# Kernel optimization log

Hardware: AMD Instinct MI355X
Metric: run time of the kernel (lower is better)

The kernel has to match this reference:

```python
import jax, jax.numpy as jnp
import numpy as np

N_NODES = 100000
N_EDGES = 1600000
IN_DIM = 128
HID = 32
HEADS = 4
NEG_SLOPE = 0.2


def gat_conv(x, src, dst, W, att_src, att_dst, bias, n_nodes, heads, out_ch):
    # x: [N, Fin], W: [Fin, heads*out_ch], att_*: [heads, out_ch], bias: [heads*out_ch]
    h = (x @ W).reshape(n_nodes, heads, out_ch)            # [N, H, C]
    a_src = jnp.einsum('nhc,hc->nh', h, att_src)           # [N, H]
    a_dst = jnp.einsum('nhc,hc->nh', h, att_dst)           # [N, H]
    e = jax.nn.leaky_relu(a_src[src] + a_dst[dst], NEG_SLOPE)  # [E, H]
    # segment softmax over incoming edges of each target node
    e_max = jax.ops.segment_max(e, dst, num_segments=n_nodes)  # [N, H]
    ex = jnp.exp(e - e_max[dst])                               # [E, H]
    denom = jax.ops.segment_sum(ex, dst, num_segments=n_nodes)  # [N, H]
    alpha = ex / denom[dst]                                     # [E, H]
    msg = h[src] * alpha[:, :, None]                            # [E, H, C]
    out = jax.ops.segment_sum(msg, dst, num_segments=n_nodes)   # [N, H, C]
    return out.reshape(n_nodes, heads * out_ch) + bias


def setup_inputs() -> dict:
    key = jax.random.key(0)
    ks = jax.random.split(key, 10)
    x = jax.random.normal(ks[0], (N_NODES, IN_DIM), dtype=jnp.float32)
    edge_index = jax.random.randint(ks[1], (2, N_EDGES), 0, N_NODES, dtype=jnp.int64) if jax.config.jax_enable_x64 else jax.random.randint(ks[1], (2, N_EDGES), 0, N_NODES, dtype=jnp.int32)
    s = 0.1
    W1 = jax.random.normal(ks[2], (IN_DIM, HEADS * HID), dtype=jnp.float32) * s
    att_src1 = jax.random.normal(ks[3], (HEADS, HID), dtype=jnp.float32) * s
    att_dst1 = jax.random.normal(ks[4], (HEADS, HID), dtype=jnp.float32) * s
    b1 = jnp.zeros((HEADS * HID,), dtype=jnp.float32)
    W2 = jax.random.normal(ks[5], (HEADS * HID, HEADS * HID), dtype=jnp.float32) * s
    att_src2 = jax.random.normal(ks[6], (HEADS, HID), dtype=jnp.float32) * s
    att_dst2 = jax.random.normal(ks[7], (HEADS, HID), dtype=jnp.float32) * s
    b2 = jnp.zeros((HEADS * HID,), dtype=jnp.float32)
    return {"x": x, "edge_index": edge_index, "W1": W1, "att_src1": att_src1,
            "att_dst1": att_dst1, "b1": b1, "W2": W2, "att_src2": att_src2,
            "att_dst2": att_dst2, "b2": b2}


def reference(x, edge_index, W1, att_src1, att_dst1, b1, W2, att_src2, att_dst2, b2):
    src, dst = edge_index[0], edge_index[1]
    x1 = jax.nn.relu(gat_conv(x, src, dst, W1, att_src1, att_dst1, b1, N_NODES, HEADS, HID))
    x2 = jax.nn.relu(gat_conv(x1, src, dst, W2, att_src2, att_dst2, b2, N_NODES, HEADS, HID))
    # [N, heads*hid, 2]
    return jnp.concatenate([x1[:, :, None], x2[:, :, None]], axis=2)
```

## Files before the change

### kernel.cpp

```cpp
#include <hip/hip_runtime.h>

#define NN 100000
#define NE 1600000
#define GEMM_GRID 1563
#define NBUK 391
#define BCAP 5120
#define PA_BLOCKS 320
#define PA_EDGES 5000
#define K1_GRID (16 + PA_BLOCKS)
#define K2_GRID (NBUK + GEMM_GRID)
#define AG1_GRID 6250
#define AGG2_GRID 12500

typedef short bf16x8 __attribute__((ext_vector_type(8)));
typedef float f32x4 __attribute__((ext_vector_type(4)));
typedef unsigned int u32;
typedef u32 u32x4 __attribute__((ext_vector_type(4)));
typedef unsigned short u16;

__device__ inline u32 bf16r(float x) {
    u32 u = __float_as_uint(x);
    return (u + 0x7FFFu + ((u >> 16) & 1u)) >> 16;
}

__device__ inline void split_pack8(const float a[8], u32 hh[4], u32 ll[4]) {
#pragma unroll
    for (int j = 0; j < 4; ++j) {
        u32 u0 = __float_as_uint(a[2 * j]);
        u32 u1 = __float_as_uint(a[2 * j + 1]);
        float l0 = a[2 * j] - __uint_as_float(u0 & 0xFFFF0000u);
        float l1 = a[2 * j + 1] - __uint_as_float(u1 & 0xFFFF0000u);
        hh[j] = (u0 >> 16) | (u1 & 0xFFFF0000u);
        ll[j] = (__float_as_uint(l0) >> 16) | (__float_as_uint(l1) & 0xFFFF0000u);
    }
}

__device__ inline void wpack_body(int idx, const float* __restrict__ W,
                                  bf16x8* __restrict__ wpH, bf16x8* __restrict__ wpL) {
    if (idx >= 2048) return;
    int lane = idx & 63, tile = idx >> 6;
    int kc = tile >> 3, ct = tile & 7;
    int col = lane & 15, kq = lane >> 4;
    int kbase = kc * 32 + kq * 8;
    float a[8];
#pragma unroll
    for (int i = 0; i < 8; ++i)
        a[i] = W[(size_t)(kbase + i) * 128 + ct * 16 + col];
    u32 hh[4], ll[4];
    split_pack8(a, hh, ll);
    wpH[tile * 64 + lane] = __builtin_bit_cast(bf16x8, (u32x4){hh[0], hh[1], hh[2], hh[3]});
    wpL[tile * 64 + lane] = __builtin_bit_cast(bf16x8, (u32x4){ll[0], ll[1], ll[2], ll[3]});
}

__global__ __launch_bounds__(256) void k1(
    const float* __restrict__ W1, bf16x8* __restrict__ wpH1, bf16x8* __restrict__ wpL1,
    const float* __restrict__ W2, bf16x8* __restrict__ wpH2, bf16x8* __restrict__ wpL2,
    const int* __restrict__ dst, const int* __restrict__ src,
    int* __restrict__ gtail, u32* __restrict__ tmp) {
    const int b = blockIdx.x;
    if (b < 8) {
        wpack_body(b * 256 + threadIdx.x, W1, wpH1, wpL1);
        return;
    } else if (b < 16) {
        wpack_body((b - 8) * 256 + threadIdx.x, W2, wpH2, wpL2);
        return;
    }
    __shared__ int lhist[NBUK], lcur[NBUK];
    const int t = threadIdx.x;
    const int e0 = (b - 16) * PA_EDGES;
    const int e1 = e0 + PA_EDGES;
    for (int i = t; i < NBUK; i += 256) lhist[i] = 0;
    __syncthreads();
    for (int e = e0 + t; e < e1; e += 256)
        atomicAdd(&lhist[dst[e] >> 8], 1);
    __syncthreads();
    for (int i = t; i < NBUK; i += 256)
        if (lhist[i] > 0) lcur[i] = atomicAdd(&gtail[i], lhist[i]);
    __syncthreads();
    for (int e = e0 + t; e < e1; e += 256) {
        int d = dst[e];
        int bb = d >> 8;
        int p = atomicAdd(&lcur[bb], 1);
        tmp[(size_t)bb * BCAP + p] = ((u32)(d & 255) << 17) | (u32)src[e];
    }
}

__device__ inline void gemm_epilogue(f32x4 acc[8], int row0, int w, int col, int kq,
                                     const float* __restrict__ atts,
                                     const float* __restrict__ attd,
                                     u16* __restrict__ hb,
                                     float* __restrict__ a_src,
                                     float* __restrict__ a_dst) {
    float as0[4], as1[4], ad0[4], ad1[4];
#pragma unroll
    for (int q = 0; q < 4; ++q) {
        as0[q] = atts[q * 32 + col];
        as1[q] = atts[q * 32 + 16 + col];
        ad0[q] = attd[q * 32 + col];
        ad1[q] = attd[q * 32 + 16 + col];
    }
#pragma unroll
    for (int r = 0; r < 4; ++r) {
        int node = row0 + w * 16 + kq * 4 + r;
        float ps[4], pd[4];
#pragma unroll
        for (int q = 0; q < 4; ++q) {
            float d0 = acc[2 * q][r], d1 = acc[2 * q + 1][r];
            ps[q] = d0 * as0[q] + d1 * as1[q];
            pd[q] = d0 * ad0[q] + d1 * ad1[q];
        }
#pragma unroll
        for (int off = 1; off < 16; off <<= 1) {
#pragma unroll
            for (int q = 0; q < 4; ++q) {
                ps[q] += __shfl_xor(ps[q], off);
                pd[q] += __shfl_xor(pd[q], off);
            }
        }
        if (node < NN) {
#pragma unroll
            for (int ct = 0; ct < 8; ++ct)
                hb[(size_t)node * 128 + ct * 16 + col] = (u16)bf16r(acc[ct][r]);
            if (col < 4) {
                float vs = col == 0 ? ps[0] : col == 1 ? ps[1] : col == 2 ? ps[2] : ps[3];
                float vd = col == 0 ? pd[0] : col == 1 ? pd[1] : col == 2 ? pd[2] : pd[3];
                a_src[node * 4 + col] = vs;
                a_dst[node * 4 + col] = vd;
            }
        }
    }
}

__global__ __launch_bounds__(256) void k2(
    const float* __restrict__ x,
    const bf16x8* __restrict__ wpH, const bf16x8* __restrict__ wpL,
    const float* __restrict__ atts, const float* __restrict__ attd,
    u16* __restrict__ hb, float* __restrict__ a_src, float* __restrict__ a_dst,
    const int* __restrict__ gtail, const u32* __restrict__ tmp,
    int* __restrict__ row_ptr, int* __restrict__ src_sorted) {
    __shared__ u32 ldata[BCAP];
    __shared__ int lh[256];
    __shared__ int lsc[256];
    const int idx = blockIdx.x;
    const int t = threadIdx.x;
    if (idx < NBUK) {
        const int g = idx;
        const int n = gtail[g];
        int acc = 0;
        for (int i = t; i < g; i += 256) acc += gtail[i];
        lsc[t] = acc;
        __syncthreads();
        for (int off = 128; off > 0; off >>= 1) {
            if (t < off) lsc[t] += lsc[t + off];
            __syncthreads();
        }
        const int ebase = lsc[0];
        lh[t] = 0;
        __syncthreads();
        for (int i = t; i < n; i += 256) {
            u32 v = tmp[(size_t)g * BCAP + i];
            ldata[i] = v;
            atomicAdd(&lh[v >> 17], 1);
        }
        __syncthreads();
        int c = lh[t];
        lsc[t] = c;
        __syncthreads();
        for (int off = 1; off < 256; off <<= 1) {
            int xv = (t >= off) ? lsc[t - off] : 0;
            __syncthreads();
            lsc[t] += xv;
            __syncthreads();
        }
        int excl = (t == 0) ? 0 : lsc[t - 1];
        int base = ebase + excl;
        lh[t] = base;
        int node = (g << 8) + t;
        if (node < NN) row_ptr[node] = base;
        if (g == NBUK - 1 && t == 0) row_ptr[NN] = ebase + n;
        __syncthreads();
        for (int i = t; i < n; i += 256) {
            u32 v = ldata[i];
            int p = atomicAdd(&lh[v >> 17], 1);
            src_sorted[p] = (int)(v & 0x1FFFFu);
        }
        return;
    }
    const int row0 = (idx - NBUK) * 64;
    const int lane = t & 63;
    const int w = t >> 6;
    const int col = lane & 15, kq = lane >> 4;
    int node_a = row0 + w * 16 + col;
    if (node_a > NN - 1) node_a = NN - 1;
    const float* xrow = x + (size_t)node_a * 128 + kq * 8;
    float a[32];
#pragma unroll
    for (int kc = 0; kc < 4; ++kc) {
        *(float4*)&a[kc * 8 + 0] = *(const float4*)(xrow + kc * 32);
        *(float4*)&a[kc * 8 + 4] = *(const float4*)(xrow + kc * 32 + 4);
    }
    f32x4 acc[8];
#pragma unroll
    for (int ct = 0; ct < 8; ++ct) acc[ct] = (f32x4){0.f, 0.f, 0.f, 0.f};
#pragma unroll
    for (int kc = 0; kc < 4; ++kc) {
        u32 hh[4], ll[4];
        split_pack8(&a[kc * 8], hh, ll);
        bf16x8 ah = __builtin_bit_cast(bf16x8, (u32x4){hh[0], hh[1], hh[2], hh[3]});
        bf16x8 al = __builtin_bit_cast(bf16x8, (u32x4){ll[0], ll[1], ll[2], ll[3]});
#pragma unroll
        for (int ct = 0; ct < 8; ++ct) {
            bf16x8 bh = wpH[(kc * 8 + ct) * 64 + lane];
            bf16x8 bl = wpL[(kc * 8 + ct) * 64 + lane];
            acc[ct] = __builtin_amdgcn_mfma_f32_16x16x32_bf16(ah, bh, acc[ct], 0, 0, 0);
            acc[ct] = __builtin_amdgcn_mfma_f32_16x16x32_bf16(al, bh, acc[ct], 0, 0, 0);
            acc[ct] = __builtin_amdgcn_mfma_f32_16x16x32_bf16(ah, bl, acc[ct], 0, 0, 0);
        }
    }
    gemm_epilogue(acc, row0, w, col, kq, atts, attd, hb, a_src, a_dst);
}

__global__ __launch_bounds__(256) void k_ag1(
    const u32* __restrict__ hb,
    const float* __restrict__ a_src, const float* __restrict__ a_dst,
    const int* __restrict__ row_ptr, const int* __restrict__ src_sorted,
    const float* __restrict__ bias1,
    const bf16x8* __restrict__ wpH2, const bf16x8* __restrict__ wpL2,
    const float* __restrict__ atts2, const float* __restrict__ attd2,
    u32* __restrict__ x1b, u16* __restrict__ hb2,
    float* __restrict__ a_src2, float* __restrict__ a_dst2) {
    __shared__ __align__(16) u32 xs[16][68];
    const int t = threadIdx.x;
    const int lane = t & 63;
    const int wv = t >> 6;
    const int q = lane >> 4;
    const int es = lane & 15;
    const int hbase = lane & 48;
    const int node0 = blockIdx.x * 16;
    const float bv0 = bias1[lane * 2], bv1 = bias1[lane * 2 + 1];
#pragma unroll 1
    for (int ni = 0; ni < 4; ++ni) {
        const int node = node0 + wv * 4 + ni;
        const int e0 = row_ptr[node], e1 = row_ptr[node + 1];
        const int emax = e1 - 1;
        const float advh = a_dst[node * 4 + q];
        float den = 0.f, a0a = 0.f, a0b = 0.f, a1a = 0.f, a1b = 0.f;
        if (e1 > e0) {
            int eidx = e0 + es;
            if (eidx > emax) eidx = emax;
            int sv = src_sorted[eidx];
            float av = a_src[sv * 4 + q];
            for (int ec = e0; ec < e1; ec += 16) {
                int cnt = e1 - ec;
                cnt = cnt < 16 ? cnt : 16;
                int eidxn = ec + 16 + es;
                if (eidxn > emax) eidxn = emax;
                int svn = src_sorted[eidxn];
                float avn = a_src[svn * 4 + q];
                float lk = av + advh;
                lk = lk > 0.f ? lk : 0.2f * lk;
                float ex = (es < cnt) ? __expf(lk - 8.f) : 0.f;
                den += ex;
                if (cnt == 16) {
                    u32 wvv[16];
#pragma unroll
                    for (int u = 0; u < 16; ++u) {
                        int su = __builtin_amdgcn_readlane(sv, u);
                        wvv[u] = hb[((size_t)su << 6) + lane];
                    }
                    float exu[16];
#pragma unroll
                    for (int u = 0; u < 16; ++u) exu[u] = __shfl(ex, hbase | u);
#pragma unroll
                    for (int u = 0; u < 16; ++u) {
                        float h0 = __uint_as_float(wvv[u] << 16);
                        float h1 = __uint_as_float(wvv[u] & 0xFFFF0000u);
                        if (u & 1) { a0b = fmaf(exu[u], h0, a0b); a1b = fmaf(exu[u], h1, a1b); }
                        else       { a0a = fmaf(exu[u], h0, a0a); a1a = fmaf(exu[u], h1, a1a); }
                    }
                } else {
                    for (int u0 = 0; u0 < cnt; u0 += 4) {
                        u32 wvv[4];
                        float exu[4];
#pragma unroll
                        for (int j = 0; j < 4; ++j) {
                            int su = __builtin_amdgcn_readlane(sv, u0 + j);
                            wvv[j] = hb[((size_t)su << 6) + lane];
                        }
#pragma unroll
                        for (int j = 0; j < 4; ++j) exu[j] = __shfl(ex, hbase | (u0 + j));
#pragma unroll
                        for (int j = 0; j < 4; ++j) {
                            float h0 = __uint_as_float(wvv[j] << 16);
                            float h1 = __uint_as_float(wvv[j] & 0xFFFF0000u);
                            if (j & 1) { a0b = fmaf(exu[j], h0, a0b); a1b = fmaf(exu[j], h1, a1b); }
                            else       { a0a = fmaf(exu[j], h0, a0a); a1a = fmaf(exu[j], h1, a1a); }
                        }
                    }
                }
                sv = svn;
                av = avn;
            }
        }
        float a0 = a0a + a0b, a1 = a1a + a1b;
#pragma unroll
        for (int m = 1; m < 16; m <<= 1) den += __shfl_xor(den, m);
        float inv = den > 0.f ? 1.f / den : 0.f;
        float r0 = fmaxf(fmaf(a0, inv, bv0), 0.f);
        float r1 = fmaxf(fmaf(a1, inv, bv1), 0.f);
        u32 pair = bf16r(r0) | (bf16r(r1) << 16);
        x1b[node * 64 + lane] = pair;
        xs[wv * 4 + ni][lane] = pair;
    }
    __syncthreads();
    const int col = lane & 15, kq = lane >> 4;
    const int ct0 = 2 * wv, ct1 = 2 * wv + 1;
    int4 aw[4];
#pragma unroll
    for (int kc = 0; kc < 4; ++kc)
        aw[kc] = *(const int4*)&xs[col][kc * 16 + kq * 4];
    f32x4 acc0 = (f32x4){0.f, 0.f, 0.f, 0.f};
    f32x4 acc1 = (f32x4){0.f, 0.f, 0.f, 0.f};
#pragma unroll
    for (int kc = 0; kc < 4; ++kc) {
        bf16x8 a = __builtin_bit_cast(bf16x8, aw[kc]);
        acc0 = __builtin_amdgcn_mfma_f32_16x16x32_bf16(a, wpH2[(kc * 8 + ct0) * 64 + lane], acc0, 0, 0, 0);
        acc0 = __builtin_amdgcn_mfma_f32_16x16x32_bf16(a, wpL2[(kc * 8 + ct0) * 64 + lane], acc0, 0, 0, 0);
        acc1 = __builtin_amdgcn_mfma_f32_16x16x32_bf16(a, wpH2[(kc * 8 + ct1) * 64 + lane], acc1, 0, 0, 0);
        acc1 = __builtin_amdgcn_mfma_f32_16x16x32_bf16(a, wpL2[(kc * 8 + ct1) * 64 + lane], acc1, 0, 0, 0);
    }
    const float as0 = atts2[wv * 32 + col], as1 = atts2[wv * 32 + 16 + col];
    const float ad0 = attd2[wv * 32 + col], ad1 = attd2[wv * 32 + 16 + col];
#pragma unroll
    for (int r = 0; r < 4; ++r) {
        int node = node0 + kq * 4 + r;
        float d0 = acc0[r], d1 = acc1[r];
        float ps = d0 * as0 + d1 * as1;
        float pd = d0 * ad0 + d1 * ad1;
#pragma unroll
        for (int off = 1; off < 16; off <<= 1) {
            ps += __shfl_xor(ps, off);
            pd += __shfl_xor(pd, off);
        }
        hb2[(size_t)node * 128 + ct0 * 16 + col] = (u16)bf16r(d0);
        hb2[(size_t)node * 128 + ct1 * 16 + col] = (u16)bf16r(d1);
        if (col == 0) {
            a_src2[node * 4 + wv] = ps;
            a_dst2[node * 4 + wv] = pd;
        }
    }
}

__global__ __launch_bounds__(256, 4) void k_agg2(
    const u32* __restrict__ hb,
    const float* __restrict__ a_src, const float* __restrict__ a_dst,
    const int* __restrict__ row_ptr, const int* __restrict__ src_sorted,
    const float* __restrict__ bias,
    const u32* __restrict__ x1b, float* __restrict__ outp) {
    const int lane = threadIdx.x & 63;
    const int node0 = blockIdx.x * 8 + (threadIdx.x >> 6) * 2;
    const int q = lane >> 4;
    const int es = lane & 15;
    const int hbase = lane & 48;
#pragma unroll
    for (int ni = 0; ni < 2; ++ni) {
        const int node = node0 + ni;
        if (node >= NN) continue;
        const int e0 = row_ptr[node], e1 = row_ptr[node + 1];
        const int emax = e1 - 1;
        const float advh = a_dst[node * 4 + q];
        float den = 0.f, a0a = 0.f, a0b = 0.f, a1a = 0.f, a1b = 0.f;
        if (e1 > e0) {
            int eidx = e0 + es;
            if (eidx > emax) eidx = emax;
            int sv = src_sorted[eidx];
            float av = a_src[sv * 4 + q];
            for (int ec = e0; ec < e1; ec += 16) {
                int cnt = e1 - ec;
                cnt = cnt < 16 ? cnt : 16;
                int eidxn = ec + 16 + es;
                if (eidxn > emax) eidxn = emax;
                int svn = src_sorted[eidxn];
                float avn = a_src[svn * 4 + q];
                float lk = av + advh;
                lk = lk > 0.f ? lk : 0.2f * lk;
                float ex = (es < cnt) ? __expf(lk - 8.f) : 0.f;
                den += ex;
                if (cnt == 16) {
                    u32 wv[16];
#pragma unroll
                    for (int u = 0; u < 16; ++u) {
                        int su = __builtin_amdgcn_readlane(sv, u);
                        wv[u] = hb[((size_t)su << 6) + lane];
                    }
                    float exu[16];
#pragma unroll
                    for (int u = 0; u < 16; ++u) exu[u] = __shfl(ex, hbase | u);
#pragma unroll
                    for (int u = 0; u < 16; ++u) {
                        float h0 = __uint_as_float(wv[u] << 16);
                        float h1 = __uint_as_float(wv[u] & 0xFFFF0000u);
                        if (u & 1) { a0b = fmaf(exu[u], h0, a0b); a1b = fmaf(exu[u], h1, a1b); }
                        else       { a0a = fmaf(exu[u], h0, a0a); a1a = fmaf(exu[u], h1, a1a); }
                    }
                } else {
                    for (int u0 = 0; u0 < cnt; u0 += 4) {
                        u32 wv[4];
                        float exu[4];
#pragma unroll
                        for (int j = 0; j < 4; ++j) {
                            int su = __builtin_amdgcn_readlane(sv, u0 + j);
                            wv[j] = hb[((size_t)su << 6) + lane];
                        }
#pragma unroll
                        for (int j = 0; j < 4; ++j) exu[j] = __shfl(ex, hbase | (u0 + j));
#pragma unroll
                        for (int j = 0; j < 4; ++j) {
                            float h0 = __uint_as_float(wv[j] << 16);
                            float h1 = __uint_as_float(wv[j] & 0xFFFF0000u);
                            if (j & 1) { a0b = fmaf(exu[j], h0, a0b); a1b = fmaf(exu[j], h1, a1b); }
                            else       { a0a = fmaf(exu[j], h0, a0a); a1a = fmaf(exu[j], h1, a1a); }
                        }
                    }
                }
                sv = svn;
                av = avn;
            }
        }
        float a0 = a0a + a0b, a1 = a1a + a1b;
#pragma unroll
        for (int m = 1; m < 16; m <<= 1) den += __shfl_xor(den, m);
        float inv = den > 0.f ? 1.f / den : 0.f;
        int c0 = lane * 2;
        float r0 = fmaxf(fmaf(a0, inv, bias[c0]), 0.f);
        float r1 = fmaxf(fmaf(a1, inv, bias[c0 + 1]), 0.f);
        u32 w1 = x1b[node * 64 + lane];
        float4 o;
        o.x = __uint_as_float(w1 << 16);
        o.y = r0;
        o.z = __uint_as_float(w1 & 0xFFFF0000u);
        o.w = r1;
        u32x4 ov = __builtin_bit_cast(u32x4, o);
        __builtin_nontemporal_store(ov,
            (u32x4*)(outp + (size_t)node * 256 + lane * 4));
    }
}


extern "C" void kernel_launch(void* const* d_in, const int* in_sizes, int n_in,
                              void* d_out, int out_size, void* d_ws, size_t ws_size,
                              hipStream_t stream) {
    const float* x   = (const float*)d_in[0];
    const int*   ei  = (const int*)d_in[1];
    const float* W1  = (const float*)d_in[2];
    const float* as1 = (const float*)d_in[3];
    const float* ad1 = (const float*)d_in[4];
    const float* b1  = (const float*)d_in[5];
    const float* W2  = (const float*)d_in[6];
    const float* as2 = (const float*)d_in[7];
    const float* ad2 = (const float*)d_in[8];
    const float* b2  = (const float*)d_in[9];
    float* out = (float*)d_out;
    const int* src = ei;
    const int* dst = ei + NE;

    char* w = (char*)d_ws;
    size_t off = 0;
    auto alloc = [&](size_t bytes) -> void* {
        void* p = w + off;
        off = (off + bytes + 255) & ~((size_t)255);
        return p;
    };
    u16* hb         = (u16*)alloc((size_t)NN * 128 * 2);
    u16* hb2        = (u16*)alloc((size_t)NN * 128 * 2);
    u32* x1b        = (u32*)alloc((size_t)NN * 64 * 4);
    float* a_src    = (float*)alloc((size_t)NN * 4 * 4);
    float* a_dst    = (float*)alloc((size_t)NN * 4 * 4);
    float* a_src2   = (float*)alloc((size_t)NN * 4 * 4);
    float* a_dst2   = (float*)alloc((size_t)NN * 4 * 4);
    int* row_ptr    = (int*)alloc((size_t)(NN + 1) * 4);
    int* gtail      = (int*)alloc(NBUK * 4);
    u32* tmp        = (u32*)alloc((size_t)NBUK * BCAP * 4);
    int* src_sorted = (int*)alloc((size_t)NE * 4);
    bf16x8* wpH1    = (bf16x8*)alloc(2048 * 16);
    bf16x8* wpL1    = (bf16x8*)alloc(2048 * 16);
    bf16x8* wpH2    = (bf16x8*)alloc(2048 * 16);
    bf16x8* wpL2    = (bf16x8*)alloc(2048 * 16);

    (void)hipMemsetAsync(gtail, 0, NBUK * 4, stream);
    k1<<<K1_GRID, 256, 0, stream>>>(W1, wpH1, wpL1, W2, wpH2, wpL2,
                                    dst, src, gtail, tmp);
    k2<<<K2_GRID, 256, 0, stream>>>(x, wpH1, wpL1, as1, ad1, hb, a_src, a_dst,
                                    gtail, tmp, row_ptr, src_sorted);
    k_ag1<<<AG1_GRID, 256, 0, stream>>>((const u32*)hb, a_src, a_dst, row_ptr,
                                        src_sorted, b1, wpH2, wpL2, as2, ad2,
                                        x1b, hb2, a_src2, a_dst2);
    k_agg2<<<AGG2_GRID, 256, 0, stream>>>((const u32*)hb2, a_src2, a_dst2,
                                          row_ptr, src_sorted, b2,
                                          (const u32*)x1b, out);
}
```

Baseline: 248.4 us.

## Make layer-2 GEMM in k_ag1 per-wave to drop block barrier

Each wave now computes the layer-2 projection for its own 4 nodes across all 8 column tiles, using a private shared-memory slice, instead of the block's 4 waves splitting column tiles over 16 shared nodes. This replaces __syncthreads with a wave-local LDS wait, so waves with short neighbor lists no longer stall on slower ones. The cost is 4x the MFMA work per wave, since 12 of the 16 MFMA rows are duplicated padding. It also means 8 accumulators, more registers, and only a quarter of lanes doing stores.

```diff
diff --git a/kernel.cpp b/kernel.cpp
--- a/kernel.cpp
+++ b/kernel.cpp
@@ -229,18 +229,18 @@
     const float* __restrict__ atts2, const float* __restrict__ attd2,
     u32* __restrict__ x1b, u16* __restrict__ hb2,
     float* __restrict__ a_src2, float* __restrict__ a_dst2) {
-    __shared__ __align__(16) u32 xs[16][68];
+    __shared__ __align__(16) u32 xs[4][16][68];
     const int t = threadIdx.x;
     const int lane = t & 63;
     const int wv = t >> 6;
     const int q = lane >> 4;
     const int es = lane & 15;
     const int hbase = lane & 48;
-    const int node0 = blockIdx.x * 16;
+    const int node0 = blockIdx.x * 16 + wv * 4;
     const float bv0 = bias1[lane * 2], bv1 = bias1[lane * 2 + 1];
 #pragma unroll 1
     for (int ni = 0; ni < 4; ++ni) {
-        const int node = node0 + wv * 4 + ni;
+        const int node = node0 + ni;
         const int e0 = row_ptr[node], e1 = row_ptr[node + 1];
         const int emax = e1 - 1;
         const float advh = a_dst[node * 4 + q];
@@ -310,43 +310,63 @@
         float r1 = fmaxf(fmaf(a1, inv, bv1), 0.f);
         u32 pair = bf16r(r0) | (bf16r(r1) << 16);
         x1b[node * 64 + lane] = pair;
-        xs[wv * 4 + ni][lane] = pair;
-    }
-    __syncthreads();
+        xs[wv][ni][lane] = pair;
+    }
+    asm volatile("s_waitcnt lgkmcnt(0)" ::: "memory");
+    __builtin_amdgcn_sched_barrier(0);
     const int col = lane & 15, kq = lane >> 4;
-    const int ct0 = 2 * wv, ct1 = 2 * wv + 1;
     int4 aw[4];
 #pragma unroll
     for (int kc = 0; kc < 4; ++kc)
-        aw[kc] = *(const int4*)&xs[col][kc * 16 + kq * 4];
-    f32x4 acc0 = (f32x4){0.f, 0.f, 0.f, 0.f};
-    f32x4 acc1 = (f32x4){0.f, 0.f, 0.f, 0.f};
+        aw[kc] = *(const int4*)&xs[wv][col & 3][kc * 16 + kq * 4];
+    f32x4 acc[8];
+#pragma unroll
+    for (int ct = 0; ct < 8; ++ct) acc[ct] = (f32x4){0.f, 0.f, 0.f, 0.f};
 #pragma unroll
     for (int kc = 0; kc < 4; ++kc) {
         bf16x8 a = __builtin_bit_cast(bf16x8, aw[kc]);
-        acc0 = __builtin_amdgcn_mfma_f32_16x16x32_bf16(a, wpH2[(kc * 8 + ct0) * 64 + lane], acc0, 0, 0, 0);
-        acc0 = __builtin_amdgcn_mfma_f32_16x16x32_bf16(a, wpL2[(kc * 8 + ct0) * 64 + lane], acc0, 0, 0, 0);
-        acc1 = __builtin_amdgcn_mfma_f32_16x16x32_bf16(a, wpH2[(kc * 8 + ct1) * 64 + lane], acc1, 0, 0, 0);
-        acc1 = __builtin_amdgcn_mfma_f32_16x16x32_bf16(a, wpL2[(kc * 8 + ct1) * 64 + lane], acc1, 0, 0, 0);
-    }
-    const float as0 = atts2[wv * 32 + col], as1 = atts2[wv * 32 + 16 + col];
-    const float ad0 = attd2[wv * 32 + col], ad1 = attd2[wv * 32 + 16 + col];
+#pragma unroll
+        for (int ct = 0; ct < 8; ++ct) {
+            acc[ct] = __builtin_amdgcn_mfma_f32_16x16x32_bf16(a, wpH2[(kc * 8 + ct) * 64 + lane], acc[ct], 0, 0, 0);
+            acc[ct] = __builtin_amdgcn_mfma_f32_16x16x32_bf16(a, wpL2[(kc * 8 + ct) * 64 + lane], acc[ct], 0, 0, 0);
+        }
+    }
+    float as0[4], as1[4], ad0[4], ad1[4];
+#pragma unroll
+    for (int qq = 0; qq < 4; ++qq) {
+        as0[qq] = atts2[qq * 32 + col];
+        as1[qq] = atts2[qq * 32 + 16 + col];
+        ad0[qq] = attd2[qq * 32 + col];
+        ad1[qq] = attd2[qq * 32 + 16 + col];
+    }
 #pragma unroll
     for (int r = 0; r < 4; ++r) {
-        int node = node0 + kq * 4 + r;
-        float d0 = acc0[r], d1 = acc1[r];
-        float ps = d0 * as0 + d1 * as1;
-        float pd = d0 * ad0 + d1 * ad1;
+        int node = node0 + r;
+        float ps[4], pd[4];
+#pragma unroll
+        for (int qq = 0; qq < 4; ++qq) {
+            float d0 = acc[2 * qq][r], d1 = acc[2 * qq + 1][r];
+            ps[qq] = d0 * as0[qq] + d1 * as1[qq];
+            pd[qq] = d0 * ad0[qq] + d1 * ad1[qq];
+        }
 #pragma unroll
         for (int off = 1; off < 16; off <<= 1) {
-            ps += __shfl_xor(ps, off);
-            pd += __shfl_xor(pd, off);
-        }
-        hb2[(size_t)node * 128 + ct0 * 16 + col] = (u16)bf16r(d0);
-        hb2[(size_t)node * 128 + ct1 * 16 + col] = (u16)bf16r(d1);
-        if (col == 0) {
-            a_src2[node * 4 + wv] = ps;
-            a_dst2[node * 4 + wv] = pd;
+#pragma unroll
+            for (int qq = 0; qq < 4; ++qq) {
+                ps[qq] += __shfl_xor(ps[qq], off);
+                pd[qq] += __shfl_xor(pd[qq], off);
+            }
+        }
+        if (kq == 0) {
+#pragma unroll
+            for (int ct = 0; ct < 8; ++ct)
+                hb2[(size_t)node * 128 + ct * 16 + col] = (u16)bf16r(acc[ct][r]);
+            if (col < 4) {
+                float vs = col == 0 ? ps[0] : col == 1 ? ps[1] : col == 2 ? ps[2] : ps[3];
+                float vd = col == 0 ? pd[0] : col == 1 ? pd[1] : col == 2 ? pd[2] : pd[3];
+                a_src2[node * 4 + col] = vs;
+                a_dst2[node * 4 + col] = vd;
+            }
         }
     }
 }
```

Measured after the change: 307.7 us. 1.24x slower.
